# Performance work log

Measured on AMD Instinct MI355X. Metric: run time of the kernel, lower is better.

The kernel has to match this reference:

```python
import jax, jax.numpy as jnp
import numpy as np

VOCAB = 29
VEC = 512      # vector_dim
HID = 1024     # hidden_size
SEN = 64       # sen_len (== seq length)
BATCH = 2048


def setup_inputs() -> dict:
    key = jax.random.key(0)
    k1, k2, k3, k4, k5, k6 = jax.random.split(key, 6)
    s_emb = 1.0
    s_ih = 1.0 / np.sqrt(HID)
    s_cls = 1.0 / np.sqrt(HID)
    return {
        "x": jax.random.randint(k1, (BATCH, SEN), 0, VOCAB, dtype=jnp.int64),
        "emb": jax.random.normal(k2, (VOCAB, VEC), dtype=jnp.float32) * s_emb,
        "W_ih": jax.random.uniform(k3, (HID, VEC), dtype=jnp.float32, minval=-s_ih, maxval=s_ih),
        "W_hh": jax.random.uniform(k4, (HID, HID), dtype=jnp.float32, minval=-s_ih, maxval=s_ih),
        "W_cls": jax.random.uniform(k5, (SEN + 1, HID), dtype=jnp.float32, minval=-s_cls, maxval=s_cls),
        "b_cls": jax.random.uniform(k6, (SEN + 1,), dtype=jnp.float32, minval=-s_cls, maxval=s_cls),
    }


def reference(x, emb, W_ih, W_hh, W_cls, b_cls):
    # Embedding lookup: [B, S, VEC]
    xe = emb[x]
    # Precompute input projections for all timesteps: [B, S, HID]
    xin = jnp.einsum("bsv,hv->bsh", xe, W_ih)

    def step(h, x_t):
        # h: [B, HID], x_t: [B, HID] (already W_ih @ x)
        h_new = jnp.tanh(x_t + h @ W_hh.T)
        return h_new, None

    h0 = jnp.zeros((x.shape[0], HID), dtype=xin.dtype)
    h_last, _ = jax.lax.scan(step, h0, jnp.swapaxes(xin, 0, 1))  # scan over S

    # h.squeeze() in torch (num_layers=1) -> [B, HID]
    logits = h_last @ W_cls.T + b_cls  # [B, SEN+1]
    return logits
```

## Files before the change

### kernel.cpp

```cpp
#include <hip/hip_runtime.h>
#include <hip/hip_bf16.h>

#define VOCAB 29
#define VEC   512
#define HID   1024
#define SEN   64
#define BATCH 2048

typedef __bf16 bf16_t;
typedef bf16_t bf16x8 __attribute__((ext_vector_type(8)));
typedef float  floatx4 __attribute__((ext_vector_type(4)));

__global__ void cvt_whh(const float* __restrict__ w, bf16_t* __restrict__ o, int n) {
    int i = blockIdx.x * blockDim.x + threadIdx.x;
    if (i < n) o[i] = (bf16_t)w[i];
}

__global__ void cvt_wcls(const float* __restrict__ w, bf16_t* __restrict__ o) {
    int i = blockIdx.x * blockDim.x + threadIdx.x;
    if (i >= 80 * HID) return;
    o[i] = (i < 65 * HID) ? (bf16_t)w[i] : (bf16_t)0.0f;
}

__global__ void proj_kernel(const float* __restrict__ emb, const float* __restrict__ wih,
                            float* __restrict__ proj) {
    int idx = blockIdx.x * blockDim.x + threadIdx.x;
    if (idx >= VOCAB * HID) return;
    int v = idx / HID, h = idx % HID;
    const float* e = emb + v * VEC;
    const float* w = wih + h * VEC;
    float s = 0.f;
    for (int k = 0; k < VEC; k += 4) {
        float4 ev = *(const float4*)(e + k);
        float4 wv = *(const float4*)(w + k);
        s += ev.x * wv.x + ev.y * wv.y + ev.z * wv.z + ev.w * wv.w;
    }
    proj[idx] = s;
}

__device__ __forceinline__ float fast_tanh(float x) {
    float e = __expf(2.0f * x);
    return 1.0f - 2.0f / (e + 1.0f);
}

__device__ __forceinline__ void load16_to_lds(const bf16_t* g, bf16_t* l) {
    auto gp = reinterpret_cast<const __attribute__((address_space(1))) unsigned int*>(
        reinterpret_cast<uintptr_t>(g));
    auto lp = reinterpret_cast<__attribute__((address_space(3))) unsigned int*>(
        static_cast<unsigned int>(reinterpret_cast<uintptr_t>(l)));
    __builtin_amdgcn_global_load_lds(gp, lp, 16, 0, 0);
}

#define BM 128
#define BN 64
#define PANEL_BLKS 16

__device__ __forceinline__ void panel_sync(int* cnt, int target, int safe) {
    __syncthreads();
    if (threadIdx.x == 0) {
        if (safe) {
            __hip_atomic_fetch_add(cnt, 1, __ATOMIC_RELEASE, __HIP_MEMORY_SCOPE_AGENT);
            while (__hip_atomic_load(cnt, __ATOMIC_ACQUIRE, __HIP_MEMORY_SCOPE_AGENT) < target)
                __builtin_amdgcn_s_sleep(1);
        } else {
            __hip_atomic_fetch_add(cnt, 1, __ATOMIC_RELAXED, __HIP_MEMORY_SCOPE_AGENT);
            while (__hip_atomic_load(cnt, __ATOMIC_RELAXED, __HIP_MEMORY_SCOPE_AGENT) < target)
                __builtin_amdgcn_s_sleep(1);
        }
    }
    __syncthreads();
    asm volatile("buffer_inv" ::: "memory");
}

#define ISSUE_AF(BUF, KBASE)                                                     \
    _Pragma("unroll")                                                            \
    for (int j = 0; j < 8; j++) {                                                \
        af[BUF][j][0] = *(const bf16x8*)(hA + ((KBASE) + j) * 32);               \
        af[BUF][j][1] = *(const bf16x8*)(hA + 16 * HID + ((KBASE) + j) * 32);    \
    }

#define COMPUTE_GROUP(BUF, KBASE)                                                \
    _Pragma("unroll")                                                            \
    for (int j = 0; j < 8; j++) {                                                \
        const int p = (4 * ((KBASE) + j) + q) ^ l7;   \
        bf16x8 b0 = *(const bf16x8*)&Bsh[l16][p * 8];                            \
        bf16x8 b1 = *(const bf16x8*)&Bsh[16 + l16][p * 8];                       \
        bf16x8 b2 = *(const bf16x8*)&Bsh[32 + l16][p * 8];                       \
        bf16x8 b3 = *(const bf16x8*)&Bsh[48 + l16][p * 8];                       \
        acc[0][0] = __builtin_amdgcn_mfma_f32_16x16x32_bf16(af[BUF][j][0], b0, acc[0][0], 0, 0, 0); \
        acc[0][1] = __builtin_amdgcn_mfma_f32_16x16x32_bf16(af[BUF][j][0], b1, acc[0][1], 0, 0, 0); \
        acc[0][2] = __builtin_amdgcn_mfma_f32_16x16x32_bf16(af[BUF][j][0], b2, acc[0][2], 0, 0, 0); \
        acc[0][3] = __builtin_amdgcn_mfma_f32_16x16x32_bf16(af[BUF][j][0], b3, acc[0][3], 0, 0, 0); \
        acc[1][0] = __builtin_amdgcn_mfma_f32_16x16x32_bf16(af[BUF][j][1], b0, acc[1][0], 0, 0, 0); \
        acc[1][1] = __builtin_amdgcn_mfma_f32_16x16x32_bf16(af[BUF][j][1], b1, acc[1][1], 0, 0, 0); \
        acc[1][2] = __builtin_amdgcn_mfma_f32_16x16x32_bf16(af[BUF][j][1], b2, acc[1][2], 0, 0, 0); \
        acc[1][3] = __builtin_amdgcn_mfma_f32_16x16x32_bf16(af[BUF][j][1], b3, acc[1][3], 0, 0, 0); \
    }

__global__ __launch_bounds__(256, 1)
void rnn_persist(const bf16_t* __restrict__ whh, const float* __restrict__ proj,
                 const int* __restrict__ x, bf16_t* hbuf, int* scnt)
{
    __shared__ __align__(16) bf16_t Bsh[BN][HID];
    __shared__ int uni_sh;

    const int tid  = threadIdx.x;
    const int m0   = blockIdx.x * BM;
    const int n0   = blockIdx.y * BN;
    const int wave = tid >> 6;
    const int lane = tid & 63;
    const int wm   = wave * 32;
    const int q    = lane >> 4;
    const int l16  = lane & 15;
    const int l7   = l16 & 7;

    int* cnt   = scnt + blockIdx.x * 64;
    int* xmask = scnt + (16 + blockIdx.x) * 64;

#pragma unroll
    for (int half = 0; half < 2; half++)
#pragma unroll
        for (int it = 0; it < 16; it++) {
            const int r = it * 4 + wave;
            load16_to_lds(whh + (n0 + r) * HID + half * 512 + (lane ^ (r & 7)) * 8,
                          &Bsh[r][half * 512 + lane * 8]);
        }

    int rowl[8];
#pragma unroll
    for (int mi = 0; mi < 2; mi++)
#pragma unroll
        for (int r = 0; r < 4; r++) rowl[mi * 4 + r] = m0 + wm + mi * 16 + q * 4 + r;

    {
        float pv[8][4];
#pragma unroll
        for (int i = 0; i < 8; i++) {
            const int tok = x[rowl[i] * SEN + 0];
            const float* pr = proj + tok * HID + n0;
#pragma unroll
            for (int ni = 0; ni < 4; ni++) pv[i][ni] = pr[ni * 16 + l16];
        }
#pragma unroll
        for (int i = 0; i < 8; i++)
#pragma unroll
            for (int ni = 0; ni < 4; ni++)
                hbuf[rowl[i] * HID + n0 + ni * 16 + l16] = (bf16_t)fast_tanh(pv[i][ni]);
    }

    __syncthreads();
    if (tid == 0) {
        const int my_xcd = (int)__builtin_amdgcn_s_getreg((3 << 11) | 20);
        __hip_atomic_fetch_or(xmask, 1 << my_xcd, __ATOMIC_RELAXED, __HIP_MEMORY_SCOPE_AGENT);
        __hip_atomic_fetch_add(cnt, 1, __ATOMIC_RELEASE, __HIP_MEMORY_SCOPE_AGENT);
        while (__hip_atomic_load(cnt, __ATOMIC_ACQUIRE, __HIP_MEMORY_SCOPE_AGENT) < PANEL_BLKS)
            __builtin_amdgcn_s_sleep(1);
        const int m = __hip_atomic_load(xmask, __ATOMIC_RELAXED, __HIP_MEMORY_SCOPE_AGENT);
        uni_sh = ((m & (m - 1)) == 0);
    }
    __syncthreads();
    asm volatile("buffer_inv" ::: "memory");
    const int safe = !uni_sh;

#pragma unroll 1
    for (int t = 1; t < SEN; t++) {
        const bf16_t* h_in  = hbuf + (size_t)((t + 1) & 1) * (BATCH * HID);
        bf16_t*       h_out = hbuf + (size_t)(t & 1) * (BATCH * HID);

        int tk[8];
#pragma unroll
        for (int i = 0; i < 8; i++) tk[i] = x[rowl[i] * SEN + t];

        floatx4 acc[2][4];
#pragma unroll
        for (int i = 0; i < 2; i++)
#pragma unroll
            for (int j = 0; j < 4; j++) acc[i][j] = (floatx4){0.f, 0.f, 0.f, 0.f};

        const bf16_t* hA = h_in + (m0 + wm + l16) * HID + q * 8;
        bf16x8 af[2][8][2];

        ISSUE_AF(0, 0)
        ISSUE_AF(1, 8)
        COMPUTE_GROUP(0, 0)
        ISSUE_AF(0, 16)
        COMPUTE_GROUP(1, 8)
        ISSUE_AF(1, 24)

        float pv[8][4];
#pragma unroll
        for (int i = 0; i < 8; i++) {
            const float* pr = proj + tk[i] * HID + n0;
#pragma unroll
            for (int ni = 0; ni < 4; ni++) pv[i][ni] = pr[ni * 16 + l16];
        }

        COMPUTE_GROUP(0, 16)
        COMPUTE_GROUP(1, 24)

#pragma unroll
        for (int mi = 0; mi < 2; mi++)
#pragma unroll
            for (int r = 0; r < 4; r++)
#pragma unroll
                for (int ni = 0; ni < 4; ni++) {
                    float v = acc[mi][ni][r] + pv[mi * 4 + r][ni];
                    h_out[rowl[mi * 4 + r] * HID + n0 + ni * 16 + l16] = (bf16_t)fast_tanh(v);
                }

        if (t < SEN - 1) panel_sync(cnt, PANEL_BLKS * (t + 1), safe);
    }
}

#undef ISSUE_AF
#undef COMPUTE_GROUP

#define CBM 128
#define CLDK 72
__global__ __launch_bounds__(256)
void classifier_mfma(const bf16_t* __restrict__ h, const bf16_t* __restrict__ wcls,
                     const float* __restrict__ bcls, float* __restrict__ out)
{
    __shared__ __align__(16) bf16_t Ash[CBM][CLDK];
    __shared__ __align__(16) bf16_t Bsh[80][CLDK];

    const int tid = threadIdx.x;
    const int m0 = blockIdx.x * CBM;
    const int wave = tid >> 6, lane = tid & 63;
    const int wm = wave * 32;
    const int q = lane >> 4, l16 = lane & 15;

    floatx4 acc[2][5];
#pragma unroll
    for (int i = 0; i < 2; i++)
#pragma unroll
        for (int j = 0; j < 5; j++) acc[i][j] = (floatx4){0.f, 0.f, 0.f, 0.f};

    for (int kk = 0; kk < HID; kk += 64) {
#pragma unroll
        for (int it = 0; it < 4; it++) {
            int idx = tid + it * 256, r = idx >> 3, c = (idx & 7) * 8;
            *(uint4*)&Ash[r][c] = *(const uint4*)&h[(m0 + r) * HID + kk + c];
        }
#pragma unroll
        for (int it = 0; it < 3; it++) {
            int idx = tid + it * 256;
            if (idx < 640) {
                int r = idx >> 3, c = (idx & 7) * 8;
                *(uint4*)&Bsh[r][c] = *(const uint4*)&wcls[r * HID + kk + c];
            }
        }
        __syncthreads();
#pragma unroll
        for (int ks = 0; ks < 64; ks += 32) {
            bf16x8 af[2], bfr[5];
#pragma unroll
            for (int mi = 0; mi < 2; mi++)
                af[mi] = *(const bf16x8*)&Ash[wm + mi * 16 + l16][ks + q * 8];
#pragma unroll
            for (int ni = 0; ni < 5; ni++)
                bfr[ni] = *(const bf16x8*)&Bsh[ni * 16 + l16][ks + q * 8];
#pragma unroll
            for (int mi = 0; mi < 2; mi++)
#pragma unroll
                for (int ni = 0; ni < 5; ni++)
                    acc[mi][ni] = __builtin_amdgcn_mfma_f32_16x16x32_bf16(
                        af[mi], bfr[ni], acc[mi][ni], 0, 0, 0);
        }
        __syncthreads();
    }

#pragma unroll
    for (int mi = 0; mi < 2; mi++) {
#pragma unroll
        for (int r = 0; r < 4; r++) {
            int gm = m0 + wm + mi * 16 + q * 4 + r;
#pragma unroll
            for (int ni = 0; ni < 5; ni++) {
                int gn = ni * 16 + l16;
                if (gn < SEN + 1)
                    out[gm * (SEN + 1) + gn] = acc[mi][ni][r] + bcls[gn];
            }
        }
    }
}

extern "C" void kernel_launch(void* const* d_in, const int* in_sizes, int n_in,
                              void* d_out, int out_size, void* d_ws, size_t ws_size,
                              hipStream_t stream)
{
    const int*   x     = (const int*)  d_in[0];
    const float* emb   = (const float*)d_in[1];
    const float* w_ih  = (const float*)d_in[2];
    const float* w_hh  = (const float*)d_in[3];
    const float* w_cls = (const float*)d_in[4];
    const float* b_cls = (const float*)d_in[5];
    float* out = (float*)d_out;

    char* ws = (char*)d_ws;
    bf16_t* whh_bf  = (bf16_t*)ws;
    float*  proj    = (float*)(ws + (2u << 20));
    bf16_t* wcls_bf = (bf16_t*)(ws + (2u << 20) + (128u << 10));
    bf16_t* h0      = (bf16_t*)(ws + (2u << 20) + (288u << 10));
    bf16_t* h1      = (bf16_t*)(ws + (6u << 20) + (288u << 10));
    int*    scnt    = (int*)   (ws + (10u << 20) + (288u << 10));

    hipMemsetAsync(scnt, 0, 32 * 64 * sizeof(int), stream);
    cvt_whh<<<(HID * HID) / 256, 256, 0, stream>>>(w_hh, whh_bf, HID * HID);
    proj_kernel<<<(VOCAB * HID + 255) / 256, 256, 0, stream>>>(emb, w_ih, proj);
    cvt_wcls<<<(80 * HID) / 256, 256, 0, stream>>>(w_cls, wcls_bf);

    dim3 grid(BATCH / BM, HID / BN);
    rnn_persist<<<grid, 256, 0, stream>>>(whh_bf, proj, x, h0, scnt);

    classifier_mfma<<<BATCH / CBM, 256, 0, stream>>>(h1, wcls_bf, b_cls, out);
}
```

Baseline: 819.7 us.

## Replace atomic counter panel barrier with per-block flag barrier and prefetch tokens

In the non-safe path, when all panel blocks share one XCD, the per-step atomic counter barrier is replaced with per-block flag stores that 16 threads poll in parallel, with no sleep. Token indices for the next step are now loaded during the current step's MMA work instead of at the top of the loop. Sched barriers pin the interleaving of A-fragment loads and MFMA groups. The aim is to shorten the inter-block synchronisation latency and hide token loads. In exchange it relies on relaxed flag ordering, and busy-spinning without sleep adds memory traffic.

```diff
diff --git a/kernel.cpp b/kernel.cpp
--- a/kernel.cpp
+++ b/kernel.cpp
@@ -54,23 +54,7 @@
 #define BM 128
 #define BN 64
 #define PANEL_BLKS 16
-
-__device__ __forceinline__ void panel_sync(int* cnt, int target, int safe) {
-    __syncthreads();
-    if (threadIdx.x == 0) {
-        if (safe) {
-            __hip_atomic_fetch_add(cnt, 1, __ATOMIC_RELEASE, __HIP_MEMORY_SCOPE_AGENT);
-            while (__hip_atomic_load(cnt, __ATOMIC_ACQUIRE, __HIP_MEMORY_SCOPE_AGENT) < target)
-                __builtin_amdgcn_s_sleep(1);
-        } else {
-            __hip_atomic_fetch_add(cnt, 1, __ATOMIC_RELAXED, __HIP_MEMORY_SCOPE_AGENT);
-            while (__hip_atomic_load(cnt, __ATOMIC_RELAXED, __HIP_MEMORY_SCOPE_AGENT) < target)
-                __builtin_amdgcn_s_sleep(1);
-        }
-    }
-    __syncthreads();
-    asm volatile("buffer_inv" ::: "memory");
-}
+#define SB() __builtin_amdgcn_sched_barrier(0)
 
 #define ISSUE_AF(BUF, KBASE)                                                     \
     _Pragma("unroll")                                                            \
@@ -116,6 +100,7 @@
 
     int* cnt   = scnt + blockIdx.x * 64;
     int* xmask = scnt + (16 + blockIdx.x) * 64;
+    int* fl    = scnt + 2048 + blockIdx.x * 64;
 
 #pragma unroll
     for (int half = 0; half < 2; half++)
@@ -133,20 +118,24 @@
         for (int r = 0; r < 4; r++) rowl[mi * 4 + r] = m0 + wm + mi * 16 + q * 4 + r;
 
     {
-        float pv[8][4];
+        float pv0[8][4];
 #pragma unroll
         for (int i = 0; i < 8; i++) {
             const int tok = x[rowl[i] * SEN + 0];
             const float* pr = proj + tok * HID + n0;
 #pragma unroll
-            for (int ni = 0; ni < 4; ni++) pv[i][ni] = pr[ni * 16 + l16];
+            for (int ni = 0; ni < 4; ni++) pv0[i][ni] = pr[ni * 16 + l16];
         }
 #pragma unroll
         for (int i = 0; i < 8; i++)
 #pragma unroll
             for (int ni = 0; ni < 4; ni++)
-                hbuf[rowl[i] * HID + n0 + ni * 16 + l16] = (bf16_t)fast_tanh(pv[i][ni]);
-    }
+                hbuf[rowl[i] * HID + n0 + ni * 16 + l16] = (bf16_t)fast_tanh(pv0[i][ni]);
+    }
+
+    int tk[8];
+#pragma unroll
+    for (int i = 0; i < 8; i++) tk[i] = x[rowl[i] * SEN + 1];
 
     __syncthreads();
     if (tid == 0) {
@@ -167,10 +156,6 @@
         const bf16_t* h_in  = hbuf + (size_t)((t + 1) & 1) * (BATCH * HID);
         bf16_t*       h_out = hbuf + (size_t)(t & 1) * (BATCH * HID);
 
-        int tk[8];
-#pragma unroll
-        for (int i = 0; i < 8; i++) tk[i] = x[rowl[i] * SEN + t];
-
         floatx4 acc[2][4];
 #pragma unroll
         for (int i = 0; i < 2; i++)
@@ -182,11 +167,6 @@
 
         ISSUE_AF(0, 0)
         ISSUE_AF(1, 8)
-        COMPUTE_GROUP(0, 0)
-        ISSUE_AF(0, 16)
-        COMPUTE_GROUP(1, 8)
-        ISSUE_AF(1, 24)
-
         float pv[8][4];
 #pragma unroll
         for (int i = 0; i < 8; i++) {
@@ -194,9 +174,23 @@
 #pragma unroll
             for (int ni = 0; ni < 4; ni++) pv[i][ni] = pr[ni * 16 + l16];
         }
-
+        SB();
+        COMPUTE_GROUP(0, 0)
+        SB();
+        ISSUE_AF(0, 16)
+        SB();
+        COMPUTE_GROUP(1, 8)
+        SB();
+        ISSUE_AF(1, 24)
+        if (t < SEN - 1) {
+#pragma unroll
+            for (int i = 0; i < 8; i++) tk[i] = x[rowl[i] * SEN + t + 1];
+        }
+        SB();
         COMPUTE_GROUP(0, 16)
+        SB();
         COMPUTE_GROUP(1, 24)
+        SB();
 
 #pragma unroll
         for (int mi = 0; mi < 2; mi++)
@@ -208,7 +202,27 @@
                     h_out[rowl[mi * 4 + r] * HID + n0 + ni * 16 + l16] = (bf16_t)fast_tanh(v);
                 }
 
-        if (t < SEN - 1) panel_sync(cnt, PANEL_BLKS * (t + 1), safe);
+        if (t < SEN - 1) {
+            __syncthreads();
+            if (safe) {
+                if (tid == 0) {
+                    __hip_atomic_fetch_add(cnt, 1, __ATOMIC_RELEASE, __HIP_MEMORY_SCOPE_AGENT);
+                    while (__hip_atomic_load(cnt, __ATOMIC_ACQUIRE, __HIP_MEMORY_SCOPE_AGENT)
+                           < PANEL_BLKS * (t + 1))
+                        __builtin_amdgcn_s_sleep(1);
+                }
+            } else {
+                if (tid == 0)
+                    __hip_atomic_store(&fl[blockIdx.y], t,
+                                       __ATOMIC_RELAXED, __HIP_MEMORY_SCOPE_AGENT);
+                if (tid < 16) {
+                    while (__hip_atomic_load(&fl[tid],
+                                             __ATOMIC_RELAXED, __HIP_MEMORY_SCOPE_AGENT) < t) {}
+                }
+            }
+            __syncthreads();
+            asm volatile("buffer_inv" ::: "memory");
+        }
     }
 }
 
@@ -305,7 +319,7 @@
     bf16_t* h1      = (bf16_t*)(ws + (6u << 20) + (288u << 10));
     int*    scnt    = (int*)   (ws + (10u << 20) + (288u << 10));
 
-    hipMemsetAsync(scnt, 0, 32 * 64 * sizeof(int), stream);
+    hipMemsetAsync(scnt, 0, 16384, stream);
     cvt_whh<<<(HID * HID) / 256, 256, 0, stream>>>(w_hh, whh_bf, HID * HID);
     proj_kernel<<<(VOCAB * HID + 255) / 256, 256, 0, stream>>>(emb, w_ih, proj);
     cvt_wcls<<<(80 * HID) / 256, 256, 0, stream>>>(w_cls, wcls_bf);
```

Measured after the change: 756.9 us. 7.7% less time.
